# Kernel tuning notes

Measured on AMD Instinct MI355X. Metric: run time of the kernel, lower is better.

Reference implementation:

```python
import jax, jax.numpy as jnp
import numpy as np

N_HEADS = 8
NODE_DIM, EDGE_DIM, TIME_DIM = 172, 172, 100
OUT_DIM = NODE_DIM + TIME_DIM  # 272, divisible by N_HEADS -> pad_dim = 0
HEAD_DIM = OUT_DIM // N_HEADS  # 34
KEY_DIM = NODE_DIM + EDGE_DIM + TIME_DIM  # 444
B, NBR = 4096, 64
LN_EPS = 1e-5


def setup_inputs() -> dict:
    key = jax.random.key(0)
    ks = jax.random.split(key, 12)
    s = 0.02
    return {
        "node_feat": jax.random.normal(ks[0], (B, NODE_DIM), jnp.float32),
        "time_feat": jax.random.normal(ks[1], (B, 1, TIME_DIM), jnp.float32),
        "edge_feat": jax.random.normal(ks[2], (B, NBR, EDGE_DIM), jnp.float32),
        "nbr_node_feat": jax.random.normal(ks[3], (B, NBR, NODE_DIM), jnp.float32),
        "nbr_time_feat": jax.random.normal(ks[4], (B, NBR, TIME_DIM), jnp.float32),
        "nbr_mask": jax.random.randint(ks[5], (B, NBR), 0, 2, jnp.int32),
        "W_Q": jax.random.normal(ks[6], (OUT_DIM, OUT_DIM), jnp.float32) * s,
        "W_KV": jax.random.normal(ks[7], (2 * OUT_DIM, KEY_DIM), jnp.float32) * s,
        "W_O": jax.random.normal(ks[8], (OUT_DIM, OUT_DIM), jnp.float32) * s,
        "b_O": jax.random.normal(ks[9], (OUT_DIM,), jnp.float32) * s,
        "ln_gamma": jnp.ones((OUT_DIM,), jnp.float32),
        "ln_beta": jnp.zeros((OUT_DIM,), jnp.float32),
    }


def reference(node_feat, time_feat, edge_feat, nbr_node_feat, nbr_time_feat,
              nbr_mask, W_Q, W_KV, W_O, b_O, ln_gamma, ln_beta):
    # Query/residual: concat node + time features -> (B, out_dim) (L=1 squeezed)
    R = jnp.concatenate([node_feat, time_feat[:, 0, :]], axis=-1)  # (B, D)
    Q = R @ W_Q.T  # (B, D)
    # Keys/values from neighbors
    Z_in = jnp.concatenate([nbr_node_feat, edge_feat, nbr_time_feat], axis=-1)  # (B,N,key_dim)
    Z = jnp.einsum('bnk,dk->bnd', Z_in, W_KV)  # (B, N, 2D)
    K, V = Z[..., :OUT_DIM], Z[..., OUT_DIM:]
    # Split heads
    Qh = Q.reshape(B, N_HEADS, HEAD_DIM)              # (B,H,d)
    Kh = K.reshape(B, NBR, N_HEADS, HEAD_DIM)         # (B,N,H,d)
    Vh = V.reshape(B, NBR, N_HEADS, HEAD_DIM)
    # Single-query attention scores: (B,H,N)
    scores = jnp.einsum('bhd,bnhd->bhn', Qh, Kh) * (HEAD_DIM ** -0.5)
    pad = (nbr_mask == 0)[:, None, :]  # (B,1,N)
    scores = jnp.where(pad, jnp.float32(-1e10), scores)
    A = jax.nn.softmax(scores, axis=-1)  # dropout is identity in eval / p=0
    O = jnp.einsum('bhn,bnhd->bhd', A, Vh).reshape(B, OUT_DIM)
    out = O @ W_O.T + b_O
    # Residual + LayerNorm
    x = out + R
    mu = jnp.mean(x, axis=-1, keepdims=True)
    var = jnp.mean(jnp.square(x - mu), axis=-1, keepdims=True)
    return (x - mu) * jax.lax.rsqrt(var + LN_EPS) * ln_gamma + ln_beta
```

## Files before the change

kernel.cpp:

```cpp
#include <hip/hip_runtime.h>
#include <hip/hip_bf16.h>
#include <string.h>

#define NROWS    4096
#define NBR      64
#define NODE_DIM 172
#define EDGE_DIM 172
#define TIME_DIM 100
#define OUT_DIM  272
#define KEY_DIM  444
#define KPAD     448
#define QK_PAD   320
#define N_HEADS  8
#define HEAD_DIM 34

typedef __attribute__((ext_vector_type(8))) short short8_t;
typedef __attribute__((ext_vector_type(4))) float f32x4;

__device__ inline short f2b(float x) {
  unsigned u = __builtin_bit_cast(unsigned, x);
  unsigned r = (u + 0x7fffu + ((u >> 16) & 1u)) >> 16;
  return (short)r;
}

__device__ inline unsigned pk2(float lo, float hi) {
  __hip_bfloat162 h = __float22bfloat162_rn(make_float2(lo, hi));
  unsigned u;
  memcpy(&u, &h, 4);
  return u;
}

template<int ROWS, int KP, int K0>
__device__ inline void pad_rows(char* A, int t) {
  constexpr int NC8 = (KP - K0) / 4;
  constexpr int LPR = 512 / ROWS;
  int r = t / LPR;
  int j = t % LPR;
  char* Arow = A + r * (2 * KP);
  int swz = (r & 7) << 4;
  uint2 zz; zz.x = 0; zz.y = 0;
  for (int c8 = j; c8 < NC8; c8 += LPR)
    *(uint2*)(Arow + ((2 * K0 + 8 * c8) ^ swz)) = zz;
}

template<int MT, int KP, int NKK>
__device__ inline void gemm_tile(const short* __restrict__ Wrow, const char* A,
                                 int lr, int lk, f32x4* acc) {
#pragma unroll
  for (int kk = 0; kk < NKK; ++kk) {
    short8_t bfrag = *(const short8_t*)(Wrow + lr * KP + kk * 32 + lk * 8);
#pragma unroll
    for (int mt = 0; mt < MT; ++mt) {
      short8_t afrag = *(const short8_t*)(A + (mt * 16 + lr) * (2 * KP) +
                                          ((kk * 64 + lk * 16) ^ ((lr & 7) << 4)));
      acc[mt] = __builtin_amdgcn_mfma_f32_16x16x32_bf16(afrag, bfrag, acc[mt], 0, 0, 0);
    }
  }
}

__global__ void convert_w(const float* __restrict__ Wkv, const float* __restrict__ Wq,
                          const float* __restrict__ Wo, short* __restrict__ wq_b,
                          short* __restrict__ wo_b, short* __restrict__ wkt,
                          short* __restrict__ wvh) {
  int i = blockIdx.x * 256 + threadIdx.x;
  if (i < OUT_DIM * QK_PAD) {
    int r = i / QK_PAD, c = i - r * QK_PAD;
    wq_b[i] = (c < OUT_DIM) ? f2b(Wq[r * OUT_DIM + c]) : (short)0;
    wo_b[i] = (c < OUT_DIM) ? f2b(Wo[r * OUT_DIM + c]) : (short)0;
  }
  if (i < N_HEADS * 448 * 64) {
    int h = i / 28672;
    int rem = i - h * 28672;
    int n = rem >> 6, d = rem & 63;
    wkt[i] = (n < KEY_DIM && d < HEAD_DIM) ? f2b(Wkv[(h * HEAD_DIM + d) * KEY_DIM + n])
                                           : (short)0;
  }
  if (i < N_HEADS * 48 * 448) {
    int h = i / 21504;
    int rem = i - h * 21504;
    int cp = rem / 448, k = rem - cp * 448;
    wvh[i] = (cp < HEAD_DIM && k < KEY_DIM)
                 ? f2b(Wkv[(OUT_DIM + h * HEAD_DIM + cp) * KEY_DIM + k])
                 : (short)0;
  }
}

__global__ __launch_bounds__(512) void q_qt(const float* __restrict__ node_feat,
                                            const float* __restrict__ time_feat,
                                            const short* __restrict__ Wq,
                                            const short* __restrict__ Wkt,
                                            short* __restrict__ Qtg) {
  __shared__ char Rlds[32 * 640];
  __shared__ char Qp[32 * 1024];
  int rb = blockIdx.x * 32, t = threadIdx.x;

  {
    int r = t >> 4, j = t & 15;
    const float4* pn = (const float4*)(node_feat + (size_t)(rb + r) * NODE_DIM);
    const float4* pt = (const float4*)(time_feat + (size_t)(rb + r) * TIME_DIM);
    float4 vn[3], vt4[2];
    int in_[3], it_[2];
#pragma unroll
    for (int i = 0; i < 3; ++i) { int f = j + 16 * i; in_[i] = f > 42 ? 42 : f; vn[i] = pn[in_[i]]; }
#pragma unroll
    for (int i = 0; i < 2; ++i) { int f = j + 16 * i; it_[i] = f > 24 ? 24 : f; vt4[i] = pt[it_[i]]; }
    char* Arow = Rlds + r * 640;
    int swz = (r & 7) << 4;
#pragma unroll
    for (int i = 0; i < 3; ++i) {
      uint2 w; w.x = pk2(vn[i].x, vn[i].y); w.y = pk2(vn[i].z, vn[i].w);
      *(uint2*)(Arow + ((8 * in_[i]) ^ swz)) = w;
    }
#pragma unroll
    for (int i = 0; i < 2; ++i) {
      uint2 w; w.x = pk2(vt4[i].x, vt4[i].y); w.y = pk2(vt4[i].z, vt4[i].w);
      *(uint2*)(Arow + ((344 + 8 * it_[i]) ^ swz)) = w;
    }
    if (j < 12) { uint2 zz; zz.x = 0; zz.y = 0; *(uint2*)(Arow + ((544 + 8 * j) ^ swz)) = zz; }
  }
  {
    uint4 zz; zz.x = 0; zz.y = 0; zz.z = 0; zz.w = 0;
    for (int i = t; i < 2048; i += 512) ((uint4*)Qp)[i] = zz;
  }
  __syncthreads();
  int wave = t >> 6, lane = t & 63, lr = lane & 15, lk = lane >> 4;
  f32x4 z = {0.f, 0.f, 0.f, 0.f};

  for (int nt = wave; nt < 17; nt += 8) {
    int nb = nt * 16;
    f32x4 acc[2] = {z, z};
    gemm_tile<2, QK_PAD, QK_PAD / 32>(Wq + nb * QK_PAD, Rlds, lr, lk, acc);
    int c = nb + lr;
    int h = c / HEAD_DIM, d = c - h * HEAD_DIM;
#pragma unroll
    for (int mt = 0; mt < 2; ++mt)
#pragma unroll
      for (int e = 0; e < 4; ++e) {
        int r = mt * 16 + lk * 4 + e;
        *(short*)(Qp + r * 1024 + h * 128 + ((2 * d) ^ ((r & 7) << 4))) = f2b(acc[mt][e]);
      }
  }
  __syncthreads();

  int h = wave;
  const short* Wh = Wkt + h * 28672;
  for (int nt = 0; nt < 28; ++nt) {
    f32x4 acc[2] = {z, z};
#pragma unroll
    for (int kk = 0; kk < 2; ++kk) {
      short8_t bfrag = *(const short8_t*)(Wh + (nt * 16 + lr) * 64 + kk * 32 + lk * 8);
#pragma unroll
      for (int mt = 0; mt < 2; ++mt) {
        short8_t afrag = *(const short8_t*)(Qp + (mt * 16 + lr) * 1024 + h * 128 +
                                            ((kk * 64 + lk * 16) ^ ((lr & 7) << 4)));
        acc[mt] = __builtin_amdgcn_mfma_f32_16x16x32_bf16(afrag, bfrag, acc[mt], 0, 0, 0);
      }
    }
#pragma unroll
    for (int mt = 0; mt < 2; ++mt)
#pragma unroll
      for (int e = 0; e < 4; ++e)
        Qtg[(size_t)(rb + mt * 16 + lk * 4 + e) * 3584 + h * 448 + nt * 16 + lr] =
            f2b(acc[mt][e] * 0.17149858514250882f);
  }
}

__global__ __launch_bounds__(512) void attn3(const float* __restrict__ nbr_node,
                                             const float* __restrict__ edge_feat,
                                             const float* __restrict__ nbr_time,
                                             const int* __restrict__ nbr_mask,
                                             const short* __restrict__ Qtg,
                                             short* __restrict__ Yh2) {
  __shared__ char Alds[64 * 896];
  __shared__ float Spart[2][64][8];
  __shared__ char Pb[16 * 128];
  int b = blockIdx.x;
  int t = threadIdx.x;

  {
    int r = t >> 3, j = t & 7;
    const float4* pn = (const float4*)(nbr_node + (size_t)b * NBR * NODE_DIM) + (size_t)r * 43;
    const float4* pe = (const float4*)(edge_feat + (size_t)b * NBR * EDGE_DIM) + (size_t)r * 43;
    const float4* pt = (const float4*)(nbr_time + (size_t)b * NBR * TIME_DIM) + (size_t)r * 25;
    float4 vn[6], ve[6], vt4[4];
    int in_[6], it_[4];
#pragma unroll
    for (int i = 0; i < 6; ++i) { int f = j + 8 * i; in_[i] = f > 42 ? 42 : f; vn[i] = pn[in_[i]]; }
#pragma unroll
    for (int i = 0; i < 6; ++i) { ve[i] = pe[in_[i]]; }
#pragma unroll
    for (int i = 0; i < 4; ++i) { int f = j + 8 * i; it_[i] = f > 24 ? 24 : f; vt4[i] = pt[it_[i]]; }
    char* Arow = Alds + r * 896;
    int swz = (r & 7) << 4;
#pragma unroll
    for (int i = 0; i < 6; ++i) {
      uint2 w; w.x = pk2(vn[i].x, vn[i].y); w.y = pk2(vn[i].z, vn[i].w);
      *(uint2*)(Arow + ((8 * in_[i]) ^ swz)) = w;
    }
#pragma unroll
    for (int i = 0; i < 6; ++i) {
      uint2 w; w.x = pk2(ve[i].x, ve[i].y); w.y = pk2(ve[i].z, ve[i].w);
      *(uint2*)(Arow + ((344 + 8 * in_[i]) ^ swz)) = w;
    }
#pragma unroll
    for (int i = 0; i < 4; ++i) {
      uint2 w; w.x = pk2(vt4[i].x, vt4[i].y); w.y = pk2(vt4[i].z, vt4[i].w);
      *(uint2*)(Arow + ((688 + 8 * it_[i]) ^ swz)) = w;
    }
    if (j == 0) { uint2 zz; zz.x = 0; zz.y = 0; *(uint2*)(Arow + (888 ^ swz)) = zz; }
  }
  __syncthreads();

  int wave = t >> 6, lane = t & 63, lr = lane & 15, lk = lane >> 4;
  f32x4 z = {0.f, 0.f, 0.f, 0.f};

  {
    int nt = wave & 3, kh = wave >> 2;
    f32x4 acc = z;
    const short* qrow = Qtg + (size_t)b * 3584 + (lr & 7) * 448;
    const char* zbase = Alds + (nt * 16 + lr) * 896;
    int swz = (lr & 7) << 4;
#pragma unroll
    for (int k7 = 0; k7 < 7; ++k7) {
      int ke = (kh * 7 + k7) * 32 + lk * 8;
      short8_t a = *(const short8_t*)(qrow + ke);
      short8_t bb = *(const short8_t*)(zbase + ((2 * ke) ^ swz));
      acc = __builtin_amdgcn_mfma_f32_16x16x32_bf16(a, bb, acc, 0, 0, 0);
    }
#pragma unroll
    for (int e = 0; e < 4; ++e) {
      int h = lk * 4 + e;
      if (h < 8) Spart[kh][nt * 16 + lr][h] = acc[e];
    }
  }
  __syncthreads();

  {
    int h = wave, n = lane;
    float s = Spart[0][n][h] + Spart[1][n][h];
    if (nbr_mask[(size_t)b * NBR + n] == 0) s = -1e10f;
    float m = s;
#pragma unroll
    for (int off = 32; off >= 1; off >>= 1) m = fmaxf(m, __shfl_xor(m, off));
    float e = __expf(s - m);
    float sum = e;
#pragma unroll
    for (int off = 32; off >= 1; off >>= 1) sum += __shfl_xor(sum, off);
    int off2 = (2 * n) ^ ((h & 7) << 4);
    *(short*)(Pb + h * 128 + off2) = f2b(e / sum);
    *(short*)(Pb + (h + 8) * 128 + off2) = 0;
  }
  __syncthreads();

  for (int vt = wave; vt < 28; vt += 8) {
    int vb = vt * 16;
    f32x4 acc = z;
    int colb = 2 * (vb + lr);
#pragma unroll
    for (int kk = 0; kk < 2; ++kk) {
      short8_t pa = *(const short8_t*)(Pb + lr * 128 +
                                       ((kk * 64 + lk * 16) ^ ((lr & 7) << 4)));
      const char* zb_base = Alds + (kk * 32 + lk * 8) * 896;
      short8_t zb;
#pragma unroll
      for (int j = 0; j < 8; ++j)
        zb[j] = *(const short*)(zb_base + j * 896 + (colb ^ (j << 4)));
      acc = __builtin_amdgcn_mfma_f32_16x16x32_bf16(pa, zb, acc, 0, 0, 0);
    }
    if (lk < 2) {
      int k = vb + lr, kk2 = k >> 5, kp = k & 31;
#pragma unroll
      for (int e = 0; e < 4; ++e) {
        int h = lk * 4 + e;
        Yh2[((size_t)(h * 14 + kk2) * 4096 + b) * 32 + kp] = f2b(acc[e]);
      }
    }
  }
}

__global__ __launch_bounds__(512) void out_ln2(const short* __restrict__ Yh2,
                                               const short* __restrict__ Wvh,
                                               const short* __restrict__ Wo,
                                               const float* __restrict__ bO,
                                               const float* __restrict__ node_feat,
                                               const float* __restrict__ time_feat,
                                               const float* __restrict__ gamma,
                                               const float* __restrict__ beta,
                                               float* __restrict__ out) {
  __shared__ char Alds[32 * 640];
  __shared__ float X[32 * 276];
  int rb = blockIdx.x * 32;
  int t = threadIdx.x;
  int wave = t >> 6, lane = t & 63, lr = lane & 15, lk = lane >> 4;
  pad_rows<32, QK_PAD, OUT_DIM>(Alds, t);
  f32x4 z = {0.f, 0.f, 0.f, 0.f};

  for (int p = wave; p < 24; p += 8) {
    int h = p / 3, nt = p - h * 3;
    f32x4 acc[2] = {z, z};
#pragma unroll
    for (int kk = 0; kk < 14; ++kk) {
      short8_t bfrag = *(const short8_t*)(Wvh + h * 21504 + (nt * 16 + lr) * 448 +
                                          kk * 32 + lk * 8);
#pragma unroll
      for (int mt = 0; mt < 2; ++mt) {
        short8_t afrag = *(const short8_t*)(
            Yh2 + ((size_t)(h * 14 + kk) * 4096 + rb + mt * 16 + lr) * 32 + lk * 8);
        acc[mt] = __builtin_amdgcn_mfma_f32_16x16x32_bf16(afrag, bfrag, acc[mt], 0, 0, 0);
      }
    }
    int cl = nt * 16 + lr;
    if (cl < HEAD_DIM) {
      int c = h * HEAD_DIM + cl;
#pragma unroll
      for (int mt = 0; mt < 2; ++mt)
#pragma unroll
        for (int e = 0; e < 4; ++e) {
          int r = mt * 16 + lk * 4 + e;
          *(short*)(Alds + r * 640 + ((2 * c) ^ ((r & 7) << 4))) = f2b(acc[mt][e]);
        }
    }
  }
  __syncthreads();

  for (int nt = wave; nt < 17; nt += 8) {
    int nb = nt * 16;
    f32x4 acc[2] = {z, z};
    gemm_tile<2, QK_PAD, QK_PAD / 32>(Wo + nb * QK_PAD, Alds, lr, lk, acc);
    int c = nb + lr;
    float bo = bO[c];
#pragma unroll
    for (int mt = 0; mt < 2; ++mt)
#pragma unroll
      for (int e = 0; e < 4; ++e) {
        int r = mt * 16 + lk * 4 + e;
        int gr = rb + r;
        float Rv = (c < NODE_DIM) ? node_feat[(size_t)gr * NODE_DIM + c]
                                  : time_feat[(size_t)gr * TIME_DIM + (c - NODE_DIM)];
        X[r * 276 + c] = acc[mt][e] + bo + Rv;
      }
  }
  __syncthreads();

  int row = t >> 4, j = t & 15;
  float s1 = 0.f, s2 = 0.f;
  for (int c = j; c < OUT_DIM; c += 16) {
    float v = X[row * 276 + c];
    s1 += v; s2 += v * v;
  }
#pragma unroll
  for (int off = 8; off >= 1; off >>= 1) {
    s1 += __shfl_xor(s1, off);
    s2 += __shfl_xor(s2, off);
  }
  float mu = s1 * (1.f / OUT_DIM);
  float var = s2 * (1.f / OUT_DIM) - mu * mu;
  float inv = rsqrtf(fmaxf(var, 0.f) + 1e-5f);
  int gr = rb + row;
  for (int c = j; c < OUT_DIM; c += 16) {
    float v = X[row * 276 + c];
    out[(size_t)gr * OUT_DIM + c] = (v - mu) * inv * gamma[c] + beta[c];
  }
}

extern "C" void kernel_launch(void* const* d_in, const int* in_sizes, int n_in,
                              void* d_out, int out_size, void* d_ws, size_t ws_size,
                              hipStream_t stream) {
  const float* node_feat = (const float*)d_in[0];
  const float* time_feat = (const float*)d_in[1];
  const float* edge_feat = (const float*)d_in[2];
  const float* nbr_node  = (const float*)d_in[3];
  const float* nbr_time  = (const float*)d_in[4];
  const int*   nbr_mask  = (const int*)d_in[5];
  const float* W_Q   = (const float*)d_in[6];
  const float* W_KV  = (const float*)d_in[7];
  const float* W_O   = (const float*)d_in[8];
  const float* b_O   = (const float*)d_in[9];
  const float* gamma = (const float*)d_in[10];
  const float* beta  = (const float*)d_in[11];
  float* out = (float*)d_out;
  char* ws = (char*)d_ws;

  short* wq_b = (short*)(ws);
  short* wo_b = (short*)(ws + 174080);
  short* wvh  = (short*)(ws + 348160);
  short* wkt  = (short*)(ws + 692224);
  short* Qtg  = (short*)(ws + 1150976);
  short* Yh2  = (short*)(ws + 30511104);

  convert_w<<<896, 256, 0, stream>>>(W_KV, W_Q, W_O, wq_b, wo_b, wkt, wvh);
  q_qt<<<NROWS / 32, 512, 0, stream>>>(node_feat, time_feat, wq_b, wkt, Qtg);
  attn3<<<NROWS, 512, 0, stream>>>(nbr_node, edge_feat, nbr_time, nbr_mask, Qtg, Yh2);
  out_ln2<<<NROWS / 32, 512, 0, stream>>>(Yh2, wvh, wo_b, b_O, node_feat, time_feat,
                                          gamma, beta, out);
}
```

Before: 191.6 us.

## Make attention kernel persistent with register prefetch of next row's neighbor features

The attention kernel becomes persistent: 512 blocks each loop over 8 batch rows. While one row is being computed out of shared memory, the next row's neighbor, edge and time features are loaded into registers. The goal is to hide global-load latency behind the MFMA and softmax work instead of relying on many short-lived blocks. In exchange, register pressure rises from holding 16 float4 prefetch values, which may cut occupancy, and there is an extra barrier per iteration.

Result: slower. 219.2 us (+14.4%).

```diff
diff --git a/kernel.cpp b/kernel.cpp
--- a/kernel.cpp
+++ b/kernel.cpp
@@ -13,6 +13,8 @@
 #define QK_PAD   320
 #define N_HEADS  8
 #define HEAD_DIM 34
+#define PBLK     512
+#define PITER    (NROWS / PBLK)
 
 typedef __attribute__((ext_vector_type(8))) short short8_t;
 typedef __attribute__((ext_vector_type(4))) float f32x4;
@@ -165,7 +167,50 @@
   }
 }
 
-__global__ __launch_bounds__(512) void attn3(const float* __restrict__ nbr_node,
+struct ZPref {
+  float4 vn[6], ve[6], vt[4];
+};
+
+__device__ inline void zload(const float* __restrict__ nbr_node,
+                             const float* __restrict__ edge_feat,
+                             const float* __restrict__ nbr_time,
+                             int b, int r, int j, ZPref& P) {
+  const float4* pn = (const float4*)(nbr_node + (size_t)b * NBR * NODE_DIM) + (size_t)r * 43;
+  const float4* pe = (const float4*)(edge_feat + (size_t)b * NBR * EDGE_DIM) + (size_t)r * 43;
+  const float4* pt = (const float4*)(nbr_time + (size_t)b * NBR * TIME_DIM) + (size_t)r * 25;
+#pragma unroll
+  for (int i = 0; i < 6; ++i) { int f = j + 8 * i; int c = f > 42 ? 42 : f; P.vn[i] = pn[c]; }
+#pragma unroll
+  for (int i = 0; i < 6; ++i) { int f = j + 8 * i; int c = f > 42 ? 42 : f; P.ve[i] = pe[c]; }
+#pragma unroll
+  for (int i = 0; i < 4; ++i) { int f = j + 8 * i; int c = f > 24 ? 24 : f; P.vt[i] = pt[c]; }
+}
+
+__device__ inline void zwrite(const ZPref& P, char* Alds, int r, int j) {
+  char* Arow = Alds + r * 896;
+  int swz = (r & 7) << 4;
+#pragma unroll
+  for (int i = 0; i < 6; ++i) {
+    int f = j + 8 * i; int c = f > 42 ? 42 : f;
+    uint2 w; w.x = pk2(P.vn[i].x, P.vn[i].y); w.y = pk2(P.vn[i].z, P.vn[i].w);
+    *(uint2*)(Arow + ((8 * c) ^ swz)) = w;
+  }
+#pragma unroll
+  for (int i = 0; i < 6; ++i) {
+    int f = j + 8 * i; int c = f > 42 ? 42 : f;
+    uint2 w; w.x = pk2(P.ve[i].x, P.ve[i].y); w.y = pk2(P.ve[i].z, P.ve[i].w);
+    *(uint2*)(Arow + ((344 + 8 * c) ^ swz)) = w;
+  }
+#pragma unroll
+  for (int i = 0; i < 4; ++i) {
+    int f = j + 8 * i; int c = f > 24 ? 24 : f;
+    uint2 w; w.x = pk2(P.vt[i].x, P.vt[i].y); w.y = pk2(P.vt[i].z, P.vt[i].w);
+    *(uint2*)(Arow + ((688 + 8 * c) ^ swz)) = w;
+  }
+  if (j == 0) { uint2 zz; zz.x = 0; zz.y = 0; *(uint2*)(Arow + (888 ^ swz)) = zz; }
+}
+
+__global__ __launch_bounds__(512) void attn4(const float* __restrict__ nbr_node,
                                              const float* __restrict__ edge_feat,
                                              const float* __restrict__ nbr_time,
                                              const int* __restrict__ nbr_mask,
@@ -174,107 +219,88 @@
   __shared__ char Alds[64 * 896];
   __shared__ float Spart[2][64][8];
   __shared__ char Pb[16 * 128];
-  int b = blockIdx.x;
   int t = threadIdx.x;
-
-  {
-    int r = t >> 3, j = t & 7;
-    const float4* pn = (const float4*)(nbr_node + (size_t)b * NBR * NODE_DIM) + (size_t)r * 43;
-    const float4* pe = (const float4*)(edge_feat + (size_t)b * NBR * EDGE_DIM) + (size_t)r * 43;
-    const float4* pt = (const float4*)(nbr_time + (size_t)b * NBR * TIME_DIM) + (size_t)r * 25;
-    float4 vn[6], ve[6], vt4[4];
-    int in_[6], it_[4];
-#pragma unroll
-    for (int i = 0; i < 6; ++i) { int f = j + 8 * i; in_[i] = f > 42 ? 42 : f; vn[i] = pn[in_[i]]; }
-#pragma unroll
-    for (int i = 0; i < 6; ++i) { ve[i] = pe[in_[i]]; }
-#pragma unroll
-    for (int i = 0; i < 4; ++i) { int f = j + 8 * i; it_[i] = f > 24 ? 24 : f; vt4[i] = pt[it_[i]]; }
-    char* Arow = Alds + r * 896;
-    int swz = (r & 7) << 4;
-#pragma unroll
-    for (int i = 0; i < 6; ++i) {
-      uint2 w; w.x = pk2(vn[i].x, vn[i].y); w.y = pk2(vn[i].z, vn[i].w);
-      *(uint2*)(Arow + ((8 * in_[i]) ^ swz)) = w;
-    }
-#pragma unroll
-    for (int i = 0; i < 6; ++i) {
-      uint2 w; w.x = pk2(ve[i].x, ve[i].y); w.y = pk2(ve[i].z, ve[i].w);
-      *(uint2*)(Arow + ((344 + 8 * in_[i]) ^ swz)) = w;
-    }
-#pragma unroll
-    for (int i = 0; i < 4; ++i) {
-      uint2 w; w.x = pk2(vt4[i].x, vt4[i].y); w.y = pk2(vt4[i].z, vt4[i].w);
-      *(uint2*)(Arow + ((688 + 8 * it_[i]) ^ swz)) = w;
-    }
-    if (j == 0) { uint2 zz; zz.x = 0; zz.y = 0; *(uint2*)(Arow + (888 ^ swz)) = zz; }
-  }
-  __syncthreads();
-
+  int sr = t >> 3, sj = t & 7;
   int wave = t >> 6, lane = t & 63, lr = lane & 15, lk = lane >> 4;
   f32x4 z = {0.f, 0.f, 0.f, 0.f};
 
-  {
-    int nt = wave & 3, kh = wave >> 2;
-    f32x4 acc = z;
-    const short* qrow = Qtg + (size_t)b * 3584 + (lr & 7) * 448;
-    const char* zbase = Alds + (nt * 16 + lr) * 896;
-    int swz = (lr & 7) << 4;
-#pragma unroll
-    for (int k7 = 0; k7 < 7; ++k7) {
-      int ke = (kh * 7 + k7) * 32 + lk * 8;
-      short8_t a = *(const short8_t*)(qrow + ke);
-      short8_t bb = *(const short8_t*)(zbase + ((2 * ke) ^ swz));
-      acc = __builtin_amdgcn_mfma_f32_16x16x32_bf16(a, bb, acc, 0, 0, 0);
-    }
-#pragma unroll
-    for (int e = 0; e < 4; ++e) {
-      int h = lk * 4 + e;
-      if (h < 8) Spart[kh][nt * 16 + lr][h] = acc[e];
-    }
-  }
-  __syncthreads();
-
-  {
-    int h = wave, n = lane;
-    float s = Spart[0][n][h] + Spart[1][n][h];
-    if (nbr_mask[(size_t)b * NBR + n] == 0) s = -1e10f;
-    float m = s;
-#pragma unroll
-    for (int off = 32; off >= 1; off >>= 1) m = fmaxf(m, __shfl_xor(m, off));
-    float e = __expf(s - m);
-    float sum = e;
-#pragma unroll
-    for (int off = 32; off >= 1; off >>= 1) sum += __shfl_xor(sum, off);
-    int off2 = (2 * n) ^ ((h & 7) << 4);
-    *(short*)(Pb + h * 128 + off2) = f2b(e / sum);
-    *(short*)(Pb + (h + 8) * 128 + off2) = 0;
-  }
-  __syncthreads();
-
-  for (int vt = wave; vt < 28; vt += 8) {
-    int vb = vt * 16;
-    f32x4 acc = z;
-    int colb = 2 * (vb + lr);
-#pragma unroll
-    for (int kk = 0; kk < 2; ++kk) {
-      short8_t pa = *(const short8_t*)(Pb + lr * 128 +
-                                       ((kk * 64 + lk * 16) ^ ((lr & 7) << 4)));
-      const char* zb_base = Alds + (kk * 32 + lk * 8) * 896;
-      short8_t zb;
-#pragma unroll
-      for (int j = 0; j < 8; ++j)
-        zb[j] = *(const short*)(zb_base + j * 896 + (colb ^ (j << 4)));
-      acc = __builtin_amdgcn_mfma_f32_16x16x32_bf16(pa, zb, acc, 0, 0, 0);
-    }
-    if (lk < 2) {
-      int k = vb + lr, kk2 = k >> 5, kp = k & 31;
+  int b = blockIdx.x;
+  ZPref P;
+  zload(nbr_node, edge_feat, nbr_time, b, sr, sj, P);
+
+  for (int it = 0; it < PITER; ++it, b += PBLK) {
+    zwrite(P, Alds, sr, sj);
+    __syncthreads();
+
+    ZPref Pn;
+    if (it + 1 < PITER)
+      zload(nbr_node, edge_feat, nbr_time, b + PBLK, sr, sj, Pn);
+
+    {
+      int nt = wave & 3, kh = wave >> 2;
+      f32x4 acc = z;
+      const short* qrow = Qtg + (size_t)b * 3584 + (lr & 7) * 448;
+      const char* zbase = Alds + (nt * 16 + lr) * 896;
+      int swz = (lr & 7) << 4;
+#pragma unroll
+      for (int k7 = 0; k7 < 7; ++k7) {
+        int ke = (kh * 7 + k7) * 32 + lk * 8;
+        short8_t a = *(const short8_t*)(qrow + ke);
+        short8_t bb = *(const short8_t*)(zbase + ((2 * ke) ^ swz));
+        acc = __builtin_amdgcn_mfma_f32_16x16x32_bf16(a, bb, acc, 0, 0, 0);
+      }
 #pragma unroll
       for (int e = 0; e < 4; ++e) {
         int h = lk * 4 + e;
-        Yh2[((size_t)(h * 14 + kk2) * 4096 + b) * 32 + kp] = f2b(acc[e]);
-      }
-    }
+        if (h < 8) Spart[kh][nt * 16 + lr][h] = acc[e];
+      }
+    }
+    __syncthreads();
+
+    {
+      int h = wave, n = lane;
+      float s = Spart[0][n][h] + Spart[1][n][h];
+      if (nbr_mask[(size_t)b * NBR + n] == 0) s = -1e10f;
+      float m = s;
+#pragma unroll
+      for (int off = 32; off >= 1; off >>= 1) m = fmaxf(m, __shfl_xor(m, off));
+      float e = __expf(s - m);
+      float sum = e;
+#pragma unroll
+      for (int off = 32; off >= 1; off >>= 1) sum += __shfl_xor(sum, off);
+      int off2 = (2 * n) ^ ((h & 7) << 4);
+      *(short*)(Pb + h * 128 + off2) = f2b(e / sum);
+      *(short*)(Pb + (h + 8) * 128 + off2) = 0;
+    }
+    __syncthreads();
+
+    for (int vt = wave; vt < 28; vt += 8) {
+      int vb = vt * 16;
+      f32x4 acc = z;
+      int colb = 2 * (vb + lr);
+#pragma unroll
+      for (int kk = 0; kk < 2; ++kk) {
+        short8_t pa = *(const short8_t*)(Pb + lr * 128 +
+                                         ((kk * 64 + lk * 16) ^ ((lr & 7) << 4)));
+        const char* zb_base = Alds + (kk * 32 + lk * 8) * 896;
+        short8_t zb;
+#pragma unroll
+        for (int jx = 0; jx < 8; ++jx)
+          zb[jx] = *(const short*)(zb_base + jx * 896 + (colb ^ (jx << 4)));
+        acc = __builtin_amdgcn_mfma_f32_16x16x32_bf16(pa, zb, acc, 0, 0, 0);
+      }
+      if (lk < 2) {
+        int k = vb + lr, kk2 = k >> 5, kp = k & 31;
+#pragma unroll
+        for (int e = 0; e < 4; ++e) {
+          int h = lk * 4 + e;
+          Yh2[((size_t)(h * 14 + kk2) * 4096 + b) * 32 + kp] = f2b(acc[e]);
+        }
+      }
+    }
+    __syncthreads();
+
+    P = Pn;
   }
 }
 
@@ -390,7 +416,7 @@
 
   convert_w<<<896, 256, 0, stream>>>(W_KV, W_Q, W_O, wq_b, wo_b, wkt, wvh);
   q_qt<<<NROWS / 32, 512, 0, stream>>>(node_feat, time_feat, wq_b, wkt, Qtg);
-  attn3<<<NROWS, 512, 0, stream>>>(nbr_node, edge_feat, nbr_time, nbr_mask, Qtg, Yh2);
+  attn4<<<PBLK, 512, 0, stream>>>(nbr_node, edge_feat, nbr_time, nbr_mask, Qtg, Yh2);
   out_ln2<<<NROWS / 32, 512, 0, stream>>>(Yh2, wvh, wo_b, b_O, node_feat, time_feat,
                                           gamma, beta, out);
 }
```

## Chunk attention over neighbors with online softmax and halve row tiles

Applied to the files above, without the earlier changes.

The attention kernel now handles the 64 neighbors in two chunks of 32 with 256 threads. It keeps an online-softmax running max and sum and rescales the Y accumulators in registers, which roughly halves LDS use per block and should let more blocks run per CU. The q_qt and out_ln2 kernels drop from 32-row to 16-row tiles, doubling their grid size so more CUs have work. In exchange there are extra syncs per chunk, more accumulator registers, and more repeated weight loads across the smaller row tiles.

After: 202.9 us. +5.9%, slower.

```diff
diff --git a/kernel.cpp b/kernel.cpp
--- a/kernel.cpp
+++ b/kernel.cpp
@@ -90,37 +90,34 @@
                                             const short* __restrict__ Wq,
                                             const short* __restrict__ Wkt,
                                             short* __restrict__ Qtg) {
-  __shared__ char Rlds[32 * 640];
-  __shared__ char Qp[32 * 1024];
-  int rb = blockIdx.x * 32, t = threadIdx.x;
-
+  __shared__ char Rlds[16 * 640];
+  __shared__ char Qp[16 * 1024];
+  int rb = blockIdx.x * 16, t = threadIdx.x;
   {
-    int r = t >> 4, j = t & 15;
+    int r = t >> 5, j = t & 31;
     const float4* pn = (const float4*)(node_feat + (size_t)(rb + r) * NODE_DIM);
     const float4* pt = (const float4*)(time_feat + (size_t)(rb + r) * TIME_DIM);
-    float4 vn[3], vt4[2];
-    int in_[3], it_[2];
-#pragma unroll
-    for (int i = 0; i < 3; ++i) { int f = j + 16 * i; in_[i] = f > 42 ? 42 : f; vn[i] = pn[in_[i]]; }
-#pragma unroll
-    for (int i = 0; i < 2; ++i) { int f = j + 16 * i; it_[i] = f > 24 ? 24 : f; vt4[i] = pt[it_[i]]; }
+    float4 vn[2], vt4;
+    int in_[2], it_;
+#pragma unroll
+    for (int i = 0; i < 2; ++i) { int f = j + 32 * i; in_[i] = f > 42 ? 42 : f; vn[i] = pn[in_[i]]; }
+    it_ = j > 24 ? 24 : j; vt4 = pt[it_];
     char* Arow = Rlds + r * 640;
     int swz = (r & 7) << 4;
 #pragma unroll
-    for (int i = 0; i < 3; ++i) {
+    for (int i = 0; i < 2; ++i) {
       uint2 w; w.x = pk2(vn[i].x, vn[i].y); w.y = pk2(vn[i].z, vn[i].w);
       *(uint2*)(Arow + ((8 * in_[i]) ^ swz)) = w;
     }
-#pragma unroll
-    for (int i = 0; i < 2; ++i) {
-      uint2 w; w.x = pk2(vt4[i].x, vt4[i].y); w.y = pk2(vt4[i].z, vt4[i].w);
-      *(uint2*)(Arow + ((344 + 8 * it_[i]) ^ swz)) = w;
+    {
+      uint2 w; w.x = pk2(vt4.x, vt4.y); w.y = pk2(vt4.z, vt4.w);
+      *(uint2*)(Arow + ((344 + 8 * it_) ^ swz)) = w;
     }
     if (j < 12) { uint2 zz; zz.x = 0; zz.y = 0; *(uint2*)(Arow + ((544 + 8 * j) ^ swz)) = zz; }
   }
   {
     uint4 zz; zz.x = 0; zz.y = 0; zz.z = 0; zz.w = 0;
-    for (int i = t; i < 2048; i += 512) ((uint4*)Qp)[i] = zz;
+    for (int i = t; i < 1024; i += 512) ((uint4*)Qp)[i] = zz;
   }
   __syncthreads();
   int wave = t >> 6, lane = t & 63, lr = lane & 15, lk = lane >> 4;
@@ -128,152 +125,166 @@
 
   for (int nt = wave; nt < 17; nt += 8) {
     int nb = nt * 16;
-    f32x4 acc[2] = {z, z};
-    gemm_tile<2, QK_PAD, QK_PAD / 32>(Wq + nb * QK_PAD, Rlds, lr, lk, acc);
+    f32x4 acc[1] = {z};
+    gemm_tile<1, QK_PAD, QK_PAD / 32>(Wq + nb * QK_PAD, Rlds, lr, lk, acc);
     int c = nb + lr;
     int h = c / HEAD_DIM, d = c - h * HEAD_DIM;
 #pragma unroll
-    for (int mt = 0; mt < 2; ++mt)
-#pragma unroll
-      for (int e = 0; e < 4; ++e) {
-        int r = mt * 16 + lk * 4 + e;
-        *(short*)(Qp + r * 1024 + h * 128 + ((2 * d) ^ ((r & 7) << 4))) = f2b(acc[mt][e]);
-      }
+    for (int e = 0; e < 4; ++e) {
+      int r = lk * 4 + e;
+      *(short*)(Qp + r * 1024 + h * 128 + ((2 * d) ^ ((r & 7) << 4))) = f2b(acc[0][e]);
+    }
   }
   __syncthreads();
 
   int h = wave;
   const short* Wh = Wkt + h * 28672;
   for (int nt = 0; nt < 28; ++nt) {
-    f32x4 acc[2] = {z, z};
+    f32x4 acc = z;
 #pragma unroll
     for (int kk = 0; kk < 2; ++kk) {
       short8_t bfrag = *(const short8_t*)(Wh + (nt * 16 + lr) * 64 + kk * 32 + lk * 8);
-#pragma unroll
-      for (int mt = 0; mt < 2; ++mt) {
-        short8_t afrag = *(const short8_t*)(Qp + (mt * 16 + lr) * 1024 + h * 128 +
-                                            ((kk * 64 + lk * 16) ^ ((lr & 7) << 4)));
-        acc[mt] = __builtin_amdgcn_mfma_f32_16x16x32_bf16(afrag, bfrag, acc[mt], 0, 0, 0);
-      }
-    }
-#pragma unroll
-    for (int mt = 0; mt < 2; ++mt)
-#pragma unroll
-      for (int e = 0; e < 4; ++e)
-        Qtg[(size_t)(rb + mt * 16 + lk * 4 + e) * 3584 + h * 448 + nt * 16 + lr] =
-            f2b(acc[mt][e] * 0.17149858514250882f);
-  }
-}
-
-__global__ __launch_bounds__(512) void attn3(const float* __restrict__ nbr_node,
+      short8_t afrag = *(const short8_t*)(Qp + lr * 1024 + h * 128 +
+                                          ((kk * 64 + lk * 16) ^ ((lr & 7) << 4)));
+      acc = __builtin_amdgcn_mfma_f32_16x16x32_bf16(afrag, bfrag, acc, 0, 0, 0);
+    }
+#pragma unroll
+    for (int e = 0; e < 4; ++e)
+      Qtg[(size_t)(rb + lk * 4 + e) * 3584 + h * 448 + nt * 16 + lr] =
+          f2b(acc[e] * 0.17149858514250882f);
+  }
+}
+
+__global__ __launch_bounds__(256) void attn5(const float* __restrict__ nbr_node,
                                              const float* __restrict__ edge_feat,
                                              const float* __restrict__ nbr_time,
                                              const int* __restrict__ nbr_mask,
                                              const short* __restrict__ Qtg,
                                              short* __restrict__ Yh2) {
-  __shared__ char Alds[64 * 896];
-  __shared__ float Spart[2][64][8];
-  __shared__ char Pb[16 * 128];
+  __shared__ char Zc[32 * 896];
+  __shared__ float Spart[2][32][8];
+  __shared__ char Pb[16 * 64];
+  __shared__ float Mh[8], Lh[8], Fh[8];
   int b = blockIdx.x;
   int t = threadIdx.x;
-
-  {
-    int r = t >> 3, j = t & 7;
-    const float4* pn = (const float4*)(nbr_node + (size_t)b * NBR * NODE_DIM) + (size_t)r * 43;
-    const float4* pe = (const float4*)(edge_feat + (size_t)b * NBR * EDGE_DIM) + (size_t)r * 43;
-    const float4* pt = (const float4*)(nbr_time + (size_t)b * NBR * TIME_DIM) + (size_t)r * 25;
-    float4 vn[6], ve[6], vt4[4];
-    int in_[6], it_[4];
-#pragma unroll
-    for (int i = 0; i < 6; ++i) { int f = j + 8 * i; in_[i] = f > 42 ? 42 : f; vn[i] = pn[in_[i]]; }
-#pragma unroll
-    for (int i = 0; i < 6; ++i) { ve[i] = pe[in_[i]]; }
-#pragma unroll
-    for (int i = 0; i < 4; ++i) { int f = j + 8 * i; it_[i] = f > 24 ? 24 : f; vt4[i] = pt[it_[i]]; }
-    char* Arow = Alds + r * 896;
-    int swz = (r & 7) << 4;
-#pragma unroll
-    for (int i = 0; i < 6; ++i) {
-      uint2 w; w.x = pk2(vn[i].x, vn[i].y); w.y = pk2(vn[i].z, vn[i].w);
-      *(uint2*)(Arow + ((8 * in_[i]) ^ swz)) = w;
-    }
-#pragma unroll
-    for (int i = 0; i < 6; ++i) {
-      uint2 w; w.x = pk2(ve[i].x, ve[i].y); w.y = pk2(ve[i].z, ve[i].w);
-      *(uint2*)(Arow + ((344 + 8 * in_[i]) ^ swz)) = w;
-    }
-#pragma unroll
-    for (int i = 0; i < 4; ++i) {
-      uint2 w; w.x = pk2(vt4[i].x, vt4[i].y); w.y = pk2(vt4[i].z, vt4[i].w);
-      *(uint2*)(Arow + ((688 + 8 * it_[i]) ^ swz)) = w;
-    }
-    if (j == 0) { uint2 zz; zz.x = 0; zz.y = 0; *(uint2*)(Arow + (888 ^ swz)) = zz; }
-  }
-  __syncthreads();
-
   int wave = t >> 6, lane = t & 63, lr = lane & 15, lk = lane >> 4;
   f32x4 z = {0.f, 0.f, 0.f, 0.f};
-
-  {
-    int nt = wave & 3, kh = wave >> 2;
-    f32x4 acc = z;
-    const short* qrow = Qtg + (size_t)b * 3584 + (lr & 7) * 448;
-    const char* zbase = Alds + (nt * 16 + lr) * 896;
-    int swz = (lr & 7) << 4;
-#pragma unroll
-    for (int k7 = 0; k7 < 7; ++k7) {
-      int ke = (kh * 7 + k7) * 32 + lk * 8;
-      short8_t a = *(const short8_t*)(qrow + ke);
-      short8_t bb = *(const short8_t*)(zbase + ((2 * ke) ^ swz));
-      acc = __builtin_amdgcn_mfma_f32_16x16x32_bf16(a, bb, acc, 0, 0, 0);
-    }
-#pragma unroll
-    for (int e = 0; e < 4; ++e) {
-      int h = lk * 4 + e;
-      if (h < 8) Spart[kh][nt * 16 + lr][h] = acc[e];
-    }
-  }
-  __syncthreads();
-
-  {
-    int h = wave, n = lane;
-    float s = Spart[0][n][h] + Spart[1][n][h];
-    if (nbr_mask[(size_t)b * NBR + n] == 0) s = -1e10f;
-    float m = s;
-#pragma unroll
-    for (int off = 32; off >= 1; off >>= 1) m = fmaxf(m, __shfl_xor(m, off));
-    float e = __expf(s - m);
-    float sum = e;
-#pragma unroll
-    for (int off = 32; off >= 1; off >>= 1) sum += __shfl_xor(sum, off);
-    int off2 = (2 * n) ^ ((h & 7) << 4);
-    *(short*)(Pb + h * 128 + off2) = f2b(e / sum);
-    *(short*)(Pb + (h + 8) * 128 + off2) = 0;
-  }
-  __syncthreads();
-
-  for (int vt = wave; vt < 28; vt += 8) {
-    int vb = vt * 16;
-    f32x4 acc = z;
-    int colb = 2 * (vb + lr);
-#pragma unroll
-    for (int kk = 0; kk < 2; ++kk) {
-      short8_t pa = *(const short8_t*)(Pb + lr * 128 +
-                                       ((kk * 64 + lk * 16) ^ ((lr & 7) << 4)));
-      const char* zb_base = Alds + (kk * 32 + lk * 8) * 896;
-      short8_t zb;
-#pragma unroll
-      for (int j = 0; j < 8; ++j)
-        zb[j] = *(const short*)(zb_base + j * 896 + (colb ^ (j << 4)));
-      acc = __builtin_amdgcn_mfma_f32_16x16x32_bf16(pa, zb, acc, 0, 0, 0);
-    }
-    if (lk < 2) {
-      int k = vb + lr, kk2 = k >> 5, kp = k & 31;
+  f32x4 accY[7] = {z, z, z, z, z, z, z};
+
+  for (int ch = 0; ch < 2; ++ch) {
+    int n0 = ch * 32;
+    {
+      int r = t >> 3, j = t & 7;
+      const float4* pn = (const float4*)(nbr_node + ((size_t)b * NBR + n0 + r) * NODE_DIM);
+      const float4* pe = (const float4*)(edge_feat + ((size_t)b * NBR + n0 + r) * EDGE_DIM);
+      const float4* pt = (const float4*)(nbr_time + ((size_t)b * NBR + n0 + r) * TIME_DIM);
+      float4 vn[6], ve[6], vt4[4];
+      int in_[6], it_[4];
+#pragma unroll
+      for (int i = 0; i < 6; ++i) { int f = j + 8 * i; in_[i] = f > 42 ? 42 : f; vn[i] = pn[in_[i]]; }
+#pragma unroll
+      for (int i = 0; i < 6; ++i) ve[i] = pe[in_[i]];
+#pragma unroll
+      for (int i = 0; i < 4; ++i) { int f = j + 8 * i; it_[i] = f > 24 ? 24 : f; vt4[i] = pt[it_[i]]; }
+      char* Arow = Zc + r * 896;
+      int swz = (r & 7) << 4;
+#pragma unroll
+      for (int i = 0; i < 6; ++i) {
+        uint2 w; w.x = pk2(vn[i].x, vn[i].y); w.y = pk2(vn[i].z, vn[i].w);
+        *(uint2*)(Arow + ((8 * in_[i]) ^ swz)) = w;
+      }
+#pragma unroll
+      for (int i = 0; i < 6; ++i) {
+        uint2 w; w.x = pk2(ve[i].x, ve[i].y); w.y = pk2(ve[i].z, ve[i].w);
+        *(uint2*)(Arow + ((344 + 8 * in_[i]) ^ swz)) = w;
+      }
+#pragma unroll
+      for (int i = 0; i < 4; ++i) {
+        uint2 w; w.x = pk2(vt4[i].x, vt4[i].y); w.y = pk2(vt4[i].z, vt4[i].w);
+        *(uint2*)(Arow + ((688 + 8 * it_[i]) ^ swz)) = w;
+      }
+      if (j == 0) { uint2 zz; zz.x = 0; zz.y = 0; *(uint2*)(Arow + (888 ^ swz)) = zz; }
+    }
+    __syncthreads();
+
+    {
+      int nt = wave & 1, kh = wave >> 1;
+      f32x4 acc = z;
+      const short* qrow = Qtg + (size_t)b * 3584 + (lr & 7) * 448;
+      const char* zbase = Zc + (nt * 16 + lr) * 896;
+      int swz = (lr & 7) << 4;
+#pragma unroll
+      for (int k7 = 0; k7 < 7; ++k7) {
+        int ke = (kh * 7 + k7) * 32 + lk * 8;
+        short8_t a = *(const short8_t*)(qrow + ke);
+        short8_t bb = *(const short8_t*)(zbase + ((2 * ke) ^ swz));
+        acc = __builtin_amdgcn_mfma_f32_16x16x32_bf16(a, bb, acc, 0, 0, 0);
+      }
 #pragma unroll
       for (int e = 0; e < 4; ++e) {
         int h = lk * 4 + e;
-        Yh2[((size_t)(h * 14 + kk2) * 4096 + b) * 32 + kp] = f2b(acc[e]);
-      }
+        if (h < 8) Spart[kh][nt * 16 + lr][h] = acc[e];
+      }
+    }
+    __syncthreads();
+
+    {
+      int h = wave * 2 + (lane >> 5);
+      int n = lane & 31;
+      float s = Spart[0][n][h] + Spart[1][n][h];
+      if (nbr_mask[(size_t)b * NBR + n0 + n] == 0) s = -1e10f;
+      float m = s;
+#pragma unroll
+      for (int off = 16; off >= 1; off >>= 1) m = fmaxf(m, __shfl_xor(m, off));
+      float mp = (ch == 0) ? -3e38f : Mh[h];
+      float mn = fmaxf(mp, m);
+      float e = __expf(s - mn);
+      float sum = e;
+#pragma unroll
+      for (int off = 16; off >= 1; off >>= 1) sum += __shfl_xor(sum, off);
+      float f = __expf(mp - mn);
+      if (n == 0) {
+        Lh[h] = (ch == 0 ? 0.f : Lh[h]) * f + sum;
+        Mh[h] = mn;
+        Fh[h] = f;
+      }
+      int off2 = (2 * n) ^ ((h & 3) << 4);
+      *(short*)(Pb + h * 64 + off2) = f2b(e);
+      *(short*)(Pb + (h + 8) * 64 + off2) = 0;
+    }
+    __syncthreads();
+
+    {
+      short8_t pa = *(const short8_t*)(Pb + lr * 64 + ((lk * 16) ^ ((lr & 3) << 4)));
+      const char* zb_base = Zc + (lk * 8) * 896;
+#pragma unroll
+      for (int s7 = 0; s7 < 7; ++s7) {
+        int vt = wave + 4 * s7;
+#pragma unroll
+        for (int e = 0; e < 4; ++e) accY[s7][e] *= Fh[(lk * 4 + e) & 7];
+        int colb = 2 * (vt * 16 + lr);
+        short8_t zb;
+#pragma unroll
+        for (int jx = 0; jx < 8; ++jx)
+          zb[jx] = *(const short*)(zb_base + jx * 896 + (colb ^ (jx << 4)));
+        accY[s7] = __builtin_amdgcn_mfma_f32_16x16x32_bf16(pa, zb, accY[s7], 0, 0, 0);
+      }
+    }
+    __syncthreads();
+  }
+
+  if (lk < 2) {
+    float inv[4];
+#pragma unroll
+    for (int e = 0; e < 4; ++e) inv[e] = 1.f / Lh[lk * 4 + e];
+#pragma unroll
+    for (int s7 = 0; s7 < 7; ++s7) {
+      int vt = wave + 4 * s7;
+      int k = vt * 16 + lr, kk2 = k >> 5, kp = k & 31;
+#pragma unroll
+      for (int e = 0; e < 4; ++e)
+        Yh2[((size_t)((lk * 4 + e) * 14 + kk2) * 4096 + b) * 32 + kp] =
+            f2b(accY[s7][e] * inv[e]);
     }
   }
 }
@@ -287,69 +298,62 @@
                                                const float* __restrict__ gamma,
                                                const float* __restrict__ beta,
                                                float* __restrict__ out) {
-  __shared__ char Alds[32 * 640];
-  __shared__ float X[32 * 276];
-  int rb = blockIdx.x * 32;
+  __shared__ char Alds[16 * 640];
+  __shared__ float X[16 * 276];
+  int rb = blockIdx.x * 16;
   int t = threadIdx.x;
   int wave = t >> 6, lane = t & 63, lr = lane & 15, lk = lane >> 4;
-  pad_rows<32, QK_PAD, OUT_DIM>(Alds, t);
+  pad_rows<16, QK_PAD, OUT_DIM>(Alds, t);
   f32x4 z = {0.f, 0.f, 0.f, 0.f};
 
   for (int p = wave; p < 24; p += 8) {
     int h = p / 3, nt = p - h * 3;
-    f32x4 acc[2] = {z, z};
+    f32x4 acc = z;
 #pragma unroll
     for (int kk = 0; kk < 14; ++kk) {
       short8_t bfrag = *(const short8_t*)(Wvh + h * 21504 + (nt * 16 + lr) * 448 +
                                           kk * 32 + lk * 8);
-#pragma unroll
-      for (int mt = 0; mt < 2; ++mt) {
-        short8_t afrag = *(const short8_t*)(
-            Yh2 + ((size_t)(h * 14 + kk) * 4096 + rb + mt * 16 + lr) * 32 + lk * 8);
-        acc[mt] = __builtin_amdgcn_mfma_f32_16x16x32_bf16(afrag, bfrag, acc[mt], 0, 0, 0);
-      }
+      short8_t afrag = *(const short8_t*)(
+          Yh2 + ((size_t)(h * 14 + kk) * 4096 + rb + lr) * 32 + lk * 8);
+      acc = __builtin_amdgcn_mfma_f32_16x16x32_bf16(afrag, bfrag, acc, 0, 0, 0);
     }
     int cl = nt * 16 + lr;
     if (cl < HEAD_DIM) {
       int c = h * HEAD_DIM + cl;
 #pragma unroll
-      for (int mt = 0; mt < 2; ++mt)
-#pragma unroll
-        for (int e = 0; e < 4; ++e) {
-          int r = mt * 16 + lk * 4 + e;
-          *(short*)(Alds + r * 640 + ((2 * c) ^ ((r & 7) << 4))) = f2b(acc[mt][e]);
-        }
+      for (int e = 0; e < 4; ++e) {
+        int r = lk * 4 + e;
+        *(short*)(Alds + r * 640 + ((2 * c) ^ ((r & 7) << 4))) = f2b(acc[e]);
+      }
     }
   }
   __syncthreads();
 
   for (int nt = wave; nt < 17; nt += 8) {
     int nb = nt * 16;
-    f32x4 acc[2] = {z, z};
-    gemm_tile<2, QK_PAD, QK_PAD / 32>(Wo + nb * QK_PAD, Alds, lr, lk, acc);
+    f32x4 acc[1] = {z};
+    gemm_tile<1, QK_PAD, QK_PAD / 32>(Wo + nb * QK_PAD, Alds, lr, lk, acc);
     int c = nb + lr;
     float bo = bO[c];
 #pragma unroll
-    for (int mt = 0; mt < 2; ++mt)
-#pragma unroll
-      for (int e = 0; e < 4; ++e) {
-        int r = mt * 16 + lk * 4 + e;
-        int gr = rb + r;
-        float Rv = (c < NODE_DIM) ? node_feat[(size_t)gr * NODE_DIM + c]
-                                  : time_feat[(size_t)gr * TIME_DIM + (c - NODE_DIM)];
-        X[r * 276 + c] = acc[mt][e] + bo + Rv;
-      }
+    for (int e = 0; e < 4; ++e) {
+      int r = lk * 4 + e;
+      int gr = rb + r;
+      float Rv = (c < NODE_DIM) ? node_feat[(size_t)gr * NODE_DIM + c]
+                                : time_feat[(size_t)gr * TIME_DIM + (c - NODE_DIM)];
+      X[r * 276 + c] = acc[0][e] + bo + Rv;
+    }
   }
   __syncthreads();
 
-  int row = t >> 4, j = t & 15;
+  int row = t >> 5, j = t & 31;
   float s1 = 0.f, s2 = 0.f;
-  for (int c = j; c < OUT_DIM; c += 16) {
+  for (int c = j; c < OUT_DIM; c += 32) {
     float v = X[row * 276 + c];
     s1 += v; s2 += v * v;
   }
 #pragma unroll
-  for (int off = 8; off >= 1; off >>= 1) {
+  for (int off = 16; off >= 1; off >>= 1) {
     s1 += __shfl_xor(s1, off);
     s2 += __shfl_xor(s2, off);
   }
@@ -357,7 +361,7 @@
   float var = s2 * (1.f / OUT_DIM) - mu * mu;
   float inv = rsqrtf(fmaxf(var, 0.f) + 1e-5f);
   int gr = rb + row;
-  for (int c = j; c < OUT_DIM; c += 16) {
+  for (int c = j; c < OUT_DIM; c += 32) {
     float v = X[row * 276 + c];
     out[(size_t)gr * OUT_DIM + c] = (v - mu) * inv * gamma[c] + beta[c];
   }
@@ -389,8 +393,8 @@
   short* Yh2  = (short*)(ws + 30511104);
 
   convert_w<<<896, 256, 0, stream>>>(W_KV, W_Q, W_O, wq_b, wo_b, wkt, wvh);
-  q_qt<<<NROWS / 32, 512, 0, stream>>>(node_feat, time_feat, wq_b, wkt, Qtg);
-  attn3<<<NROWS, 512, 0, stream>>>(nbr_node, edge_feat, nbr_time, nbr_mask, Qtg, Yh2);
-  out_ln2<<<NROWS / 32, 512, 0, stream>>>(Yh2, wvh, wo_b, b_O, node_feat, time_feat,
+  q_qt<<<NROWS / 16, 512, 0, stream>>>(node_feat, time_feat, wq_b, wkt, Qtg);
+  attn5<<<NROWS, 256, 0, stream>>>(nbr_node, edge_feat, nbr_time, nbr_mask, Qtg, Yh2);
+  out_ln2<<<NROWS / 16, 512, 0, stream>>>(Yh2, wvh, wo_b, b_O, node_feat, time_feat,
                                           gamma, beta, out);
 }
```
